# Kernel tuning notes

Measured on AMD Instinct MI355X. Metric: run time of the kernel, lower is better.

## Reference

```python
import jax, jax.numpy as jnp
import numpy as np

N, U, K, S = 1024, 64, 2, 2        # nodes, rnn_units, max_diffusion_step, num_supports
Q = S * K + 1                       # diffusion matrices (incl. identity)
B, T, H = 64, 12, 12                # batch, seq_len, horizon
IN, OUT, L = 1, 1, 2                # input_dim, output_dim, num_rnn_layers


def setup_inputs() -> dict:
    key = jax.random.key(0)
    ks = jax.random.split(key, 16)

    def glorot(k, shape):
        fan = shape[0] + shape[-1]
        return jax.random.normal(k, shape, jnp.float32) * np.float32(np.sqrt(2.0 / fan))

    # random-walk supports from a random dense adjacency (DCRNN: transpose of D^-1 A)
    adj = jax.random.uniform(ks[0], (N, N), jnp.float32)
    rw = lambda a: a / a.sum(axis=1, keepdims=True)
    supports = jnp.stack([rw(adj).T, rw(adj.T).T])  # (S, N, N)

    inputs = jax.random.normal(ks[1], (B, N * IN, T), jnp.float32)

    p = {}
    i = 2
    for pre, ind in (("enc", IN), ("dec", OUT)):
        for l in range(L):
            f = (ind if l == 0 else U) + U
            p[f"{pre}_gw{l}"] = glorot(ks[i], (Q * f, 2 * U)); i += 1
            p[f"{pre}_gb{l}"] = jnp.ones((2 * U,), jnp.float32)   # GRU gate bias init 1.0
            p[f"{pre}_cw{l}"] = glorot(ks[i], (Q * f, U)); i += 1
            p[f"{pre}_cb{l}"] = jnp.zeros((U,), jnp.float32)
    p["proj_w"] = glorot(ks[i], (U, OUT))
    p["proj_b"] = jnp.zeros((OUT,), jnp.float32)
    return {"inputs": inputs, "supports": supports, **p}


def _diffusion(x, supports):
    # x: (B, N, F) -> (B, N, Q*F); Chebyshev-style recurrence as in DCGRUCell._gconv
    mats = [x]
    for s in range(S):
        A = supports[s]
        x0 = x
        x1 = jnp.einsum('nm,bmf->bnf', A, x0)
        mats.append(x1)
        for _ in range(2, K + 1):
            x2 = 2.0 * jnp.einsum('nm,bmf->bnf', A, x1) - x0
            mats.append(x2)
            x0, x1 = x1, x2
    return jnp.concatenate(mats, axis=-1)


def _cell(x, h, supports, gw, gb, cw, cb):
    # x: (B,N,Fin), h: (B,N,U)
    ru = jax.nn.sigmoid(_diffusion(jnp.concatenate([x, h], -1), supports) @ gw + gb)
    r, u = ru[..., :U], ru[..., U:]
    c = jnp.tanh(_diffusion(jnp.concatenate([x, r * h], -1), supports) @ cw + cb)
    return u * h + (1.0 - u) * c


def reference(inputs, supports,
              enc_gw0, enc_gb0, enc_cw0, enc_cb0,
              enc_gw1, enc_gb1, enc_cw1, enc_cb1,
              dec_gw0, dec_gb0, dec_cw0, dec_cb0,
              dec_gw1, dec_gb1, dec_cw1, dec_cb1,
              proj_w, proj_b):
    enc = [(enc_gw0, enc_gb0, enc_cw0, enc_cb0), (enc_gw1, enc_gb1, enc_cw1, enc_cb1)]
    dec = [(dec_gw0, dec_gb0, dec_cw0, dec_cb0), (dec_gw1, dec_gb1, dec_cw1, dec_cb1)]

    x_seq = inputs.reshape(B, N, IN, T).transpose(3, 0, 1, 2)  # (T, B, N, IN)
    h0 = jnp.zeros((L, B, N, U), inputs.dtype)

    def enc_step(h, x):
        out, hs = x, []
        for l in range(L):
            hn = _cell(out, h[l], supports, *enc[l])
            hs.append(hn)
            out = hn
        return jnp.stack(hs), None

    hT, _ = jax.lax.scan(enc_step, h0, x_seq)

    def dec_step(carry, _):
        h, xin = carry
        out, hs = xin, []
        for l in range(L):
            hn = _cell(out, h[l], supports, *dec[l])
            hs.append(hn)
            out = hn
        proj = out @ proj_w + proj_b          # (B, N, OUT)
        return (jnp.stack(hs), proj), proj.reshape(B, N * OUT)

    go = jnp.zeros((B, N, OUT), inputs.dtype)
    _, outs = jax.lax.scan(dec_step, (hT, go), None, length=H)
    return outs  # (H, B, N*OUT)
```

## Files before the change

### kernel.cpp

```cpp
#include <hip/hip_runtime.h>

typedef _Float16 f16;
typedef _Float16 f16x4 __attribute__((ext_vector_type(4)));
typedef _Float16 f16x8 __attribute__((ext_vector_type(8)));
typedef float    f32x4 __attribute__((ext_vector_type(4)));

#define NN 1024
#define NT 12
#define NHOR 12
#define ROWS (NN*64)
#define MATH (1024*1024)
static const long SLOT = (long)NN*4096;

__device__ __forceinline__ int sw4(int row){ return (row ^ (row>>2)) & 3; }

__device__ __forceinline__ int ilvpos(int k){
  int r = k & 31;
  return (k & ~31) + ((r & 12) << 1) + (r & 3) + ((r & 16) >> 2);
}

__device__ __forceinline__ void gld(const f16* g, f16* l){
  __builtin_amdgcn_global_load_lds((const __attribute__((address_space(1))) void*)g,
                                   (__attribute__((address_space(3))) void*)l, 16, 0, 0);
}

template<int NR>
__device__ __forceinline__ void stage(f16* lds, const f16* src, int ldk, int k0, int tid){
  #pragma unroll
  for (int ic=0; ic<NR/64; ++ic){
    const int c = tid + ic*256;
    const int row = c>>2, c4 = c&3;
    const f16* g = src + (long)row*ldk + k0 + ((c4 ^ sw4(row))<<3);
    gld(g, lds + c*8);
  }
}
__device__ __forceinline__ f16x8 fragI(const f16* lds, int row, int rq){
  return *(const f16x8*)&lds[row*32 + ((rq ^ sw4(row))<<3)];
}
__device__ __forceinline__ f16x8 fragN(const f16* lds, int row, int lk){
  const int s = sw4(row);
  const int cl = (lk>>3) ^ s, ch = (2|(lk>>3)) ^ s;
  f16x4 lo = *(const f16x4*)&lds[row*32 + (cl<<3) + (lk&7)];
  f16x4 hi = *(const f16x4*)&lds[row*32 + (ch<<3) + (lk&7)];
  f16x8 r; r[0]=lo[0];r[1]=lo[1];r[2]=lo[2];r[3]=lo[3];
  r[4]=hi[0];r[5]=hi[1];r[6]=hi[2];r[7]=hi[3];
  return r;
}

struct DiffP {
  const f16* W; const f16* Y0; const f16* Y1;
  f16* out0; f16* out1;
  int nct0; int mode_x; int wsq;
};

__global__ __launch_bounds__(256) void gemm_diff(DiffP p) {
  __shared__ f16 L[4][8192];
  const int tid=threadIdx.x, l=tid&63, w=tid>>6;
  const int ro=l&15, rq=l>>4;
  const int rt = blockIdx.x, ct = blockIdx.y;
  const int part = (ct >= p.nct0) ? 1 : 0;
  const int ctl  = part ? ct - p.nct0 : ct;
  const f16* Wb = p.W + (long)rt*(128*1024);
  const f16* Yb = (part ? p.Y1 : p.Y0) + (long)ctl*(128*1024);
  const int wm=(w>>1)*64, wc=(w&1)*64;
  const int ra=tid>>2, pa=tid&3, rb=(tid+256)>>2, pb2=tid&3;
  const long sa = (long)ra*1024 + ((pa ^ (ra&3))<<3);
  const long sb = (long)rb*1024 + ((pb2 ^ (rb&3))<<3);
  const int da = tid*8, db = (tid+256)*8;
  f32x4 acc[4][4] = {};
  auto STAGE = [&](int tt){
    f16* Lr = L[tt&3]; const int k0 = tt*32;
    gld(Wb+k0+sa, Lr+da);      gld(Wb+k0+sb, Lr+db);
    gld(Yb+k0+sa, Lr+4096+da); gld(Yb+k0+sb, Lr+4096+db);
  };
  STAGE(0); STAGE(1);
  asm volatile("s_waitcnt vmcnt(4)" ::: "memory");
  __builtin_amdgcn_s_barrier();
  __builtin_amdgcn_sched_barrier(0);
  for (int t=0; t<32; ++t) {
    const f16* Lw = L[t&3];
    const f16* Ly = Lw + 4096;
    if (t+2 < 32) STAGE(t+2);
    f16x8 b[4];
    #pragma unroll
    for (int j=0;j<4;j++){ const int r=wc+j*16+ro; b[j]=*(const f16x8*)&Ly[r*32+((rq^(r&3))<<3)]; }
    __builtin_amdgcn_s_setprio(1);
    if (!p.wsq) {
      #pragma unroll
      for (int i=0;i<4;i++){
        const int r=wm+i*16+ro;
        const f16x8 a = *(const f16x8*)&Lw[r*32+((rq^(r&3))<<3)];
        #pragma unroll
        for (int j=0;j<4;j++)
          acc[i][j]=__builtin_amdgcn_mfma_f32_16x16x32_f16(a,b[j],acc[i][j],0,0,0);
      }
    } else {
      #pragma unroll
      for (int i=0;i<4;i++){
        const int r=wm+i*16+ro;
        const f16x8 a = *(const f16x8*)&Lw[r*32+((rq^(r&3))<<3)];
        #pragma unroll
        for (int j=0;j<4;j++)
          acc[i][j]=__builtin_amdgcn_mfma_f32_16x16x32_f16(b[j],a,acc[i][j],0,0,0);
      }
    }
    __builtin_amdgcn_s_setprio(0);
    if (t==31) break;
    if (t<29) { asm volatile("s_waitcnt vmcnt(4)" ::: "memory"); }
    else      { asm volatile("s_waitcnt vmcnt(0)" ::: "memory"); }
    __builtin_amdgcn_s_barrier();
    __builtin_amdgcn_sched_barrier(0);
  }
  if (p.wsq) {
    #pragma unroll
    for (int i=0;i<4;i++){
      const int n = rt*128 + wm + i*16 + ro;
      #pragma unroll
      for (int j=0;j<4;j++){
        const int m0 = ct*128 + wc + j*16 + rq*4;
        f16x4 sv;
        #pragma unroll
        for (int e=0;e<4;e++) sv[e] = (f16)(2.f*acc[i][j][e] - ((n==m0+e)?1.f:0.f));
        *(f16x4*)&p.out0[(long)n*1024 + m0] = sv;
      }
    }
    return;
  }
  f16* ob = part ? p.out1 : p.out0;
  const int mode = part ? p.mode_x : 0;
  #pragma unroll
  for (int i=0;i<4;i++){
    #pragma unroll
    for (int e=0;e<4;e++){
      const int c = rt*128 + wm + i*16 + rq*4 + e;
      const int q = c>>10, nn = c&1023;
      #pragma unroll
      for (int j=0;j<4;j++){
        const f16 v = (f16)acc[i][j][e];
        if (mode==0) {
          ob[(long)q*SLOT + (long)nn*4096 + (long)ctl*128 + wc + j*16 + ro] = v;
        } else {
          const int bul = wc + j*16 + ro;
          if (bul < 64) ob[(long)q*ROWS + nn*64 + bul] = v;
        }
      }
    }
  }
}

struct Tab5 { const f16* p[5]; };
struct CellP {
  Tab5 ta, tb, xq;
  const f16 *wa, *wb, *wx0;
  const float* bias;
  const float* h32in;
  f16* rh; f16* rhhat; float* u32;
  float* h32io; f16* h16io; f16* hhat;
  int nseg, xf1;
};

template<int O, int GATE>
__global__ __launch_bounds__(256) void cell_gemm(CellP p) {
  constexpr int FC = O/32;
  __shared__ f16 As[128*32];
  __shared__ f16 Bs[O*32];
  const int tid=threadIdx.x, l=tid&63, w=tid>>6;
  const int rq=l>>4, ro=l&15, lk=rq*4;
  const int wm=(w>>1)*64, wc=(w&1)*(O/2);
  f32x4 acc[4][FC] = {};
  const long r0 = (long)blockIdx.x*128;
  const int Ktot = p.nseg*320;
  for (int kg=0; kg<Ktot; kg+=32) {
    const int seg = (kg>=320) ? 1 : 0;
    const int kk  = kg - seg*320;
    const int q = kk>>6, kq = kk&63;
    const f16* asrc = (seg ? p.tb.p[q] : p.ta.p[q]) + r0*64;
    const f16* wsrc = seg ? p.wb : p.wa;
    stage<128>(As, asrc, 64, kq, tid);
    stage<O>(Bs, wsrc, 320, kk, tid);
    __syncthreads();
    f16x8 a[4], b[FC];
    #pragma unroll
    for (int i=0;i<4;i++) a[i] = fragN(As, wm + i*16 + ro, lk);
    #pragma unroll
    for (int j=0;j<FC;j++) b[j] = fragI(Bs, wc + j*16 + ro, rq);
    #pragma unroll
    for (int i=0;i<4;i++)
      #pragma unroll
      for (int j=0;j<FC;j++)
        acc[i][j] = __builtin_amdgcn_mfma_f32_16x16x32_f16(a[i], b[j], acc[i][j], 0,0,0);
    __syncthreads();
  }
  #pragma unroll
  for (int i=0;i<4;i++) {
    #pragma unroll
    for (int e=0;e<4;e++) {
      const long rg = r0 + wm + i*16 + rq*4 + e;
      const int bb = (int)(rg & 63), nn2 = (int)(rg >> 6);
      const long hcol = (long)ilvpos(nn2);
      float xv[5];
      if (p.xf1) {
        #pragma unroll
        for (int q2=0;q2<5;q2++) xv[q2] = (float)p.xq.p[q2][rg];
      }
      #pragma unroll
      for (int j=0;j<FC;j++) {
        const int col = wc + j*16 + ro;
        float v = acc[i][j][e] + p.bias[col];
        if (p.xf1) {
          #pragma unroll
          for (int q2=0;q2<5;q2++) v += xv[q2] * (float)p.wx0[q2*O + col];
        }
        if (GATE) {
          const float s = 1.f/(1.f + __expf(-v));
          if (col < 64) {
            const float rhv = s * p.h32in[rg*64 + col];
            p.rh[rg*64 + col] = (f16)rhv;
            p.rhhat[((long)bb*64 + col)*1024 + hcol] = (f16)rhv;
          } else {
            p.u32[rg*64 + (col-64)] = s;
          }
        } else {
          const float cc = tanhf(v);
          const float u  = p.u32[rg*64 + col];
          const float h  = p.h32io[rg*64 + col];
          const float hn = u*h + (1.f-u)*cc;
          p.h32io[rg*64 + col] = hn;
          p.h16io[rg*64 + col] = (f16)hn;
          p.hhat[((long)bb*64 + col)*1024 + hcol] = (f16)hn;
        }
      }
    }
  }
}

__global__ __launch_bounds__(256) void k_transpose(const f16* in, f16* out, int R, int C) {
  __shared__ f16 T[64*66];
  const long rb = (long)blockIdx.x*64, cb = (long)blockIdx.y*64;
  const int t = threadIdx.x;
  #pragma unroll
  for (int it=0; it<2; ++it) {
    const int r = (t>>3) + it*32, c8 = (t&7)*8;
    f16x8 v = *(const f16x8*)(in + (rb+r)*C + cb + c8);
    *(f16x8*)&T[r*66 + c8] = v;
  }
  __syncthreads();
  #pragma unroll
  for (int it=0; it<2; ++it) {
    const int c = (t>>3) + it*32, r8 = (t&7)*8;
    f16x8 v;
    #pragma unroll
    for (int j=0;j<8;j++) v[j] = T[(r8+j)*66 + c];
    *(f16x8*)(out + (cb+c)*R + rb + r8) = v;
  }
}

__global__ void k_cast_sup(const float* s, f16* o) {
  long i = (long)blockIdx.x*256 + threadIdx.x;
  if (i < 2LL*MATH) o[i] = (f16)s[i];
}

__global__ void k_ilv(const f16* in, f16* out) {
  int i = blockIdx.x*256 + threadIdx.x;
  if (i >= MATH) return;
  int r = i>>10, k = i&1023;
  out[(long)r*1024 + ilvpos(k)] = in[i];
}

__global__ void k_pack_x(const float* in, f16* xe, f16* xet) {
  int i = blockIdx.x*256 + threadIdx.x;
  if (i >= NT*ROWS) return;
  int t = i / ROWS, r = i % ROWS, n = r>>6, b = r&63;
  float v = in[(long)b*NN*NT + (long)n*NT + t];
  xe[i] = (f16)v;
  xet[(long)t*262144 + (long)b*1024 + ilvpos(n)] = (f16)v;
}

__global__ void k_split_w_t(const float* src, f16* wh_t, f16* wxA, int f, int xf, int O) {
  int i = blockIdx.x*256 + threadIdx.x;
  if (i >= 5*f*O) return;
  int o = i % O, rr = i / O, q = rr / f, ff = rr % f;
  f16 v = (f16)src[i];
  if (ff < xf) {
    if (xf == 1) wxA[q*O + o] = v;
    else         wxA[(long)o*320 + q*64 + ilvpos(ff)] = v;
  } else {
    wh_t[(long)o*320 + q*64 + ilvpos(ff - xf)] = v;
  }
}

__global__ void k_proj(const float* h32, const float* pw, const float* pb,
                       float* out, f16* xdec, f16* xdect) {
  int r = blockIdx.x*256 + threadIdx.x;
  if (r >= ROWS) return;
  float acc = pb[0];
  const float* hp = h32 + (long)r*64;
  #pragma unroll
  for (int k=0;k<64;k++) acc += hp[k]*pw[k];
  int n = r>>6, b = r&63;
  out[(long)b*NN + n] = acc;
  xdec[r] = (f16)acc;
  xdect[(long)b*1024 + ilvpos(n)] = (f16)acc;
}

extern "C" void kernel_launch(void* const* d_in, const int* in_sizes, int n_in,
                              void* d_out, int out_size, void* d_ws, size_t ws_size,
                              hipStream_t stream) {
  (void)in_sizes; (void)n_in; (void)out_size; (void)ws_size;
  const float* inputs = (const float*)d_in[0];
  const float* sup    = (const float*)d_in[1];
  const float* gwp[4] = {(const float*)d_in[2], (const float*)d_in[6], (const float*)d_in[10], (const float*)d_in[14]};
  const float* gbp[4] = {(const float*)d_in[3], (const float*)d_in[7], (const float*)d_in[11], (const float*)d_in[15]};
  const float* cwp[4] = {(const float*)d_in[4], (const float*)d_in[8], (const float*)d_in[12], (const float*)d_in[16]};
  const float* cbp[4] = {(const float*)d_in[5], (const float*)d_in[9], (const float*)d_in[13], (const float*)d_in[17]};
  const float* pw = (const float*)d_in[18];
  const float* pb = (const float*)d_in[19];
  float* out = (float*)d_out;

  char* base = (char*)d_ws; size_t off = 0;
  auto alloc = [&](size_t bytes)->void* { void* p = base + off; off += (bytes + 255) & ~(size_t)255; return p; };
  f16* W16int = (f16*)alloc(4LL*MATH*2);
  f16* xenc   = (f16*)alloc((long)NT*ROWS*2);
  f16* xet    = (f16*)alloc((long)NT*262144*2);
  f16* xdec   = (f16*)alloc((long)ROWS*2);
  f16* xdect  = (f16*)alloc(262144L*2);
  f16*  h16[2]  = {(f16*)alloc((long)ROWS*64*2),  (f16*)alloc((long)ROWS*64*2)};
  f16*  hh[2]   = {(f16*)alloc(4096L*1024*2),     (f16*)alloc(4096L*1024*2)};
  float* h32[2] = {(float*)alloc((long)ROWS*64*4), (float*)alloc((long)ROWS*64*4)};
  float* u32 = (float*)alloc((long)ROWS*64*4);
  f16* rh    = (f16*)alloc((long)ROWS*64*2);
  f16* rhh   = (f16*)alloc(4096L*1024*2);
  f16* Dh    = (f16*)alloc(4*SLOT*2);
  f16* Dx    = (f16*)alloc(4*SLOT*2);
  f16* Dx0   = (f16*)alloc(4LL*ROWS*2);
  f16 *gwh[4], *gwx[4], *cwh[4], *cwx[4];
  for (int i=0;i<4;i++) {
    gwh[i]=(f16*)alloc(128L*320*2); gwx[i]=(f16*)alloc(128L*320*2);
    cwh[i]=(f16*)alloc(64L*320*2);  cwx[i]=(f16*)alloc(64L*320*2);
  }

  hipMemsetAsync(h16[0], 0, (long)ROWS*64*2, stream);
  hipMemsetAsync(h16[1], 0, (long)ROWS*64*2, stream);
  hipMemsetAsync(hh[0],  0, 4096L*1024*2, stream);
  hipMemsetAsync(hh[1],  0, 4096L*1024*2, stream);
  hipMemsetAsync(h32[0], 0, (long)ROWS*64*4, stream);
  hipMemsetAsync(h32[1], 0, (long)ROWS*64*4, stream);
  hipMemsetAsync(xdec,   0, (long)ROWS*2, stream);
  hipMemsetAsync(xdect,  0, 262144L*2, stream);
  hipMemsetAsync(xet,    0, (long)NT*262144*2, stream);

  f16* tmpA   = Dh;
  f16* tmpAt  = Dh + 2L*MATH;
  f16* tmpAti = Dh + 4L*MATH;
  f16* tmpSq  = Dh + 5L*MATH;
  k_cast_sup<<<(2*MATH+255)/256, 256, 0, stream>>>(sup, tmpA);
  for (int s=0;s<2;s++) {
    k_transpose<<<dim3(16,16),256,0,stream>>>(tmpA + (long)s*MATH, tmpAt + (long)s*MATH, 1024, 1024);
    k_ilv<<<4096,256,0,stream>>>(tmpA + (long)s*MATH, W16int + (long)(2*s)*MATH);
  }
  for (int s=0;s<2;s++) {
    k_ilv<<<4096,256,0,stream>>>(tmpAt + (long)s*MATH, tmpAti);
    DiffP mp{};
    mp.W = W16int + (long)(2*s)*MATH; mp.Y0 = tmpAti; mp.Y1 = tmpAti;
    mp.out0 = tmpSq; mp.nct0 = 8; mp.wsq = 1;
    gemm_diff<<<dim3(8,8),256,0,stream>>>(mp);
    k_ilv<<<4096,256,0,stream>>>(tmpSq, W16int + (long)(2*s+1)*MATH);
  }
  k_pack_x<<<(NT*ROWS+255)/256,256,0,stream>>>(inputs, xenc, xet);
  const int fs[4]  = {65,128,65,128};
  const int xfs[4] = {1,64,1,64};
  for (int i=0;i<4;i++) {
    k_split_w_t<<<(5*fs[i]*128+255)/256,256,0,stream>>>(gwp[i], gwh[i], gwx[i], fs[i], xfs[i], 128);
    k_split_w_t<<<(5*fs[i]*64 +255)/256,256,0,stream>>>(cwp[i], cwh[i], cwx[i], fs[i], xfs[i], 64);
  }

  auto run_cell = [&](const f16* xraw, const f16* xhat, int xf,
                      f16* h16c, f16* hhatc, float* h32c, int wi) {
    DiffP dp{};
    dp.W = W16int; dp.Y0 = hhatc; dp.out0 = Dh; dp.nct0 = 32; dp.wsq = 0;
    int gy;
    if (xf == 64) { dp.Y1 = xhat; dp.out1 = Dx;  dp.mode_x = 0; gy = 64; }
    else          { dp.Y1 = xhat; dp.out1 = Dx0; dp.mode_x = 2; gy = 33; }
    gemm_diff<<<dim3(32, gy), 256, 0, stream>>>(dp);
    CellP gp{};
    gp.ta.p[0] = h16c; for (int q=1;q<5;q++) gp.ta.p[q] = Dh + (long)(q-1)*SLOT;
    gp.wa = gwh[wi]; gp.bias = gbp[wi];
    gp.h32in = h32c; gp.rh = rh; gp.rhhat = rhh; gp.u32 = u32;
    if (xf == 64) {
      gp.nseg = 2; gp.xf1 = 0;
      gp.tb.p[0] = xraw; for (int q=1;q<5;q++) gp.tb.p[q] = Dx + (long)(q-1)*SLOT;
      gp.wb = gwx[wi];
    } else {
      gp.nseg = 1; gp.xf1 = 1;
      gp.xq.p[0] = xraw; for (int q=1;q<5;q++) gp.xq.p[q] = Dx0 + (long)(q-1)*ROWS;
      gp.wx0 = gwx[wi];
    }
    cell_gemm<128,1><<<512, 256, 0, stream>>>(gp);
    DiffP dp2{};
    dp2.W = W16int; dp2.Y0 = rhh; dp2.Y1 = rhh; dp2.out0 = Dh; dp2.nct0 = 32; dp2.wsq = 0;
    gemm_diff<<<dim3(32, 32), 256, 0, stream>>>(dp2);
    CellP cp{};
    cp.ta.p[0] = rh; for (int q=1;q<5;q++) cp.ta.p[q] = Dh + (long)(q-1)*SLOT;
    cp.wa = cwh[wi]; cp.bias = cbp[wi];
    cp.u32 = u32; cp.h32io = h32c; cp.h16io = h16c; cp.hhat = hhatc;
    if (xf == 64) {
      cp.nseg = 2; cp.xf1 = 0;
      cp.tb.p[0] = xraw; for (int q=1;q<5;q++) cp.tb.p[q] = Dx + (long)(q-1)*SLOT;
      cp.wb = cwx[wi];
    } else {
      cp.nseg = 1; cp.xf1 = 1;
      cp.xq.p[0] = xraw; for (int q=1;q<5;q++) cp.xq.p[q] = Dx0 + (long)(q-1)*ROWS;
      cp.wx0 = cwx[wi];
    }
    cell_gemm<64,0><<<512, 256, 0, stream>>>(cp);
  };

  for (int t=0;t<NT;t++) {
    run_cell(xenc + (long)t*ROWS, xet + (long)t*262144, 1, h16[0], hh[0], h32[0], 0);
    run_cell(h16[0], hh[0],                            64, h16[1], hh[1], h32[1], 1);
  }
  for (int s=0;s<NHOR;s++) {
    run_cell(xdec,   xdect,   1, h16[0], hh[0], h32[0], 2);
    run_cell(h16[0], hh[0],  64, h16[1], hh[1], h32[1], 3);
    k_proj<<<ROWS/256, 256, 0, stream>>>(h32[1], pw, pb, out + (long)s*ROWS, xdec, xdect);
  }
}
```

Measured before the change: 11.95 ms.

## Pipeline cell GEMM with 4-buffer async LDS staging and deepen diffusion prefetch

The cell GEMM used one LDS buffer with a synchronous stage, syncthreads, compute, syncthreads loop. It now keeps four LDS buffers, stays three tiles ahead with global_load_lds, and waits only for the oldest tile using counted vmcnt waits and raises wave priority around the MFMA block. The diffusion GEMM's prefetch distance goes from two tiles to three using its existing four buffers. The aim is to hide global-load latency behind MFMA work, at the cost of four times the cell-GEMM LDS footprint, which may reduce occupancy.

```diff
diff --git a/kernel.cpp b/kernel.cpp
--- a/kernel.cpp
+++ b/kernel.cpp
@@ -22,6 +22,14 @@
 __device__ __forceinline__ void gld(const f16* g, f16* l){
   __builtin_amdgcn_global_load_lds((const __attribute__((address_space(1))) void*)g,
                                    (__attribute__((address_space(3))) void*)l, 16, 0, 0);
+}
+
+template<int N> __device__ __forceinline__ void vmwait(){
+  if constexpr (N==0)      asm volatile("s_waitcnt vmcnt(0)" ::: "memory");
+  else if constexpr (N==3) asm volatile("s_waitcnt vmcnt(3)" ::: "memory");
+  else if constexpr (N==4) asm volatile("s_waitcnt vmcnt(4)" ::: "memory");
+  else if constexpr (N==6) asm volatile("s_waitcnt vmcnt(6)" ::: "memory");
+  else if constexpr (N==8) asm volatile("s_waitcnt vmcnt(8)" ::: "memory");
 }
 
 template<int NR>
@@ -63,9 +71,9 @@
   const f16* Wb = p.W + (long)rt*(128*1024);
   const f16* Yb = (part ? p.Y1 : p.Y0) + (long)ctl*(128*1024);
   const int wm=(w>>1)*64, wc=(w&1)*64;
-  const int ra=tid>>2, pa=tid&3, rb=(tid+256)>>2, pb2=tid&3;
+  const int ra=tid>>2, pa=tid&3, rb=(tid+256)>>2;
   const long sa = (long)ra*1024 + ((pa ^ (ra&3))<<3);
-  const long sb = (long)rb*1024 + ((pb2 ^ (rb&3))<<3);
+  const long sb = (long)rb*1024 + ((pa ^ (rb&3))<<3);
   const int da = tid*8, db = (tid+256)*8;
   f32x4 acc[4][4] = {};
   auto STAGE = [&](int tt){
@@ -73,14 +81,14 @@
     gld(Wb+k0+sa, Lr+da);      gld(Wb+k0+sb, Lr+db);
     gld(Yb+k0+sa, Lr+4096+da); gld(Yb+k0+sb, Lr+4096+db);
   };
-  STAGE(0); STAGE(1);
-  asm volatile("s_waitcnt vmcnt(4)" ::: "memory");
+  STAGE(0); STAGE(1); STAGE(2);
+  vmwait<8>();
   __builtin_amdgcn_s_barrier();
   __builtin_amdgcn_sched_barrier(0);
   for (int t=0; t<32; ++t) {
     const f16* Lw = L[t&3];
     const f16* Ly = Lw + 4096;
-    if (t+2 < 32) STAGE(t+2);
+    if (t+3 < 32) STAGE(t+3);
     f16x8 b[4];
     #pragma unroll
     for (int j=0;j<4;j++){ const int r=wc+j*16+ro; b[j]=*(const f16x8*)&Ly[r*32+((rq^(r&3))<<3)]; }
@@ -106,8 +114,9 @@
     }
     __builtin_amdgcn_s_setprio(0);
     if (t==31) break;
-    if (t<29) { asm volatile("s_waitcnt vmcnt(4)" ::: "memory"); }
-    else      { asm volatile("s_waitcnt vmcnt(0)" ::: "memory"); }
+    if (t+3 < 32)      vmwait<8>();
+    else if (t+2 < 32) vmwait<4>();
+    else               vmwait<0>();
     __builtin_amdgcn_s_barrier();
     __builtin_amdgcn_sched_barrier(0);
   }
@@ -162,34 +171,49 @@
 template<int O, int GATE>
 __global__ __launch_bounds__(256) void cell_gemm(CellP p) {
   constexpr int FC = O/32;
-  __shared__ f16 As[128*32];
-  __shared__ f16 Bs[O*32];
+  constexpr int LPS = 2 + O/64;
+  __shared__ f16 As[4][128*32];
+  __shared__ f16 Bs[4][O*32];
   const int tid=threadIdx.x, l=tid&63, w=tid>>6;
   const int rq=l>>4, ro=l&15, lk=rq*4;
   const int wm=(w>>1)*64, wc=(w&1)*(O/2);
   f32x4 acc[4][FC] = {};
   const long r0 = (long)blockIdx.x*128;
-  const int Ktot = p.nseg*320;
-  for (int kg=0; kg<Ktot; kg+=32) {
-    const int seg = (kg>=320) ? 1 : 0;
-    const int kk  = kg - seg*320;
+  const int nt = p.nseg*10;
+  auto STG = [&](int t){
+    const int kg = t*32;
+    const int seg = (kg>=320)?1:0;
+    const int kk = kg - seg*320;
     const int q = kk>>6, kq = kk&63;
     const f16* asrc = (seg ? p.tb.p[q] : p.ta.p[q]) + r0*64;
     const f16* wsrc = seg ? p.wb : p.wa;
-    stage<128>(As, asrc, 64, kq, tid);
-    stage<O>(Bs, wsrc, 320, kk, tid);
-    __syncthreads();
+    stage<128>(As[t&3], asrc, 64, kq, tid);
+    stage<O>(Bs[t&3], wsrc, 320, kk, tid);
+  };
+  STG(0); STG(1); STG(2);
+  vmwait<2*LPS>();
+  __builtin_amdgcn_s_barrier();
+  __builtin_amdgcn_sched_barrier(0);
+  for (int t=0; t<nt; ++t) {
+    if (t+3 < nt) STG(t+3);
     f16x8 a[4], b[FC];
     #pragma unroll
-    for (int i=0;i<4;i++) a[i] = fragN(As, wm + i*16 + ro, lk);
-    #pragma unroll
-    for (int j=0;j<FC;j++) b[j] = fragI(Bs, wc + j*16 + ro, rq);
+    for (int i=0;i<4;i++) a[i] = fragN(As[t&3], wm + i*16 + ro, lk);
+    #pragma unroll
+    for (int j=0;j<FC;j++) b[j] = fragI(Bs[t&3], wc + j*16 + ro, rq);
+    __builtin_amdgcn_s_setprio(1);
     #pragma unroll
     for (int i=0;i<4;i++)
       #pragma unroll
       for (int j=0;j<FC;j++)
         acc[i][j] = __builtin_amdgcn_mfma_f32_16x16x32_f16(a[i], b[j], acc[i][j], 0,0,0);
-    __syncthreads();
+    __builtin_amdgcn_s_setprio(0);
+    if (t == nt-1) break;
+    if (t+3 < nt)      vmwait<2*LPS>();
+    else if (t+2 < nt) vmwait<LPS>();
+    else               vmwait<0>();
+    __builtin_amdgcn_s_barrier();
+    __builtin_amdgcn_sched_barrier(0);
   }
   #pragma unroll
   for (int i=0;i<4;i++) {
```

Measured after the change: 11.98 ms. About the same (+0.3%).
